# Kernel tuning notes

Hardware: AMD Instinct MI355X
Metric: run time of the kernel (lower is better)

## Reference

```python
import jax, jax.numpy as jnp
import numpy as np

B, T, W, H = 4, 4096, 1024, 8
BW = W // H  # block width


@jax.custom_vjp
def sqrt_bound(x):
    return jnp.sqrt(x)

def _sb_fwd(x):
    return jnp.sqrt(x), x

def _sb_bwd(x, g):
    return (g / jnp.sqrt(jnp.clip(4.0 * x, 1e-6)),)

sqrt_bound.defvjp(_sb_fwd, _sb_bwd)


def block_diag_linear(x, w, b):
    # x: [B,T,W] -> [B,T,H,BW]; w: [H,BW,BW]; b: [H,BW]
    xb = x.reshape(x.shape[0], x.shape[1], H, BW)
    y = jnp.einsum('bthi,hij->bthj', xb, w) + b
    return y.reshape(x.shape)


def setup_inputs() -> dict:
    key = jax.random.key(0)
    k1, k2, k3, k4 = jax.random.split(key, 4)
    x = jax.random.normal(k1, (B, T, W), dtype=jnp.float32)
    segment_pos = jnp.broadcast_to(jnp.arange(T, dtype=jnp.int32)[None, :], (B, T))
    std = 1.0 / np.sqrt(BW)
    w_in = std * jax.random.normal(k2, (H, BW, BW), dtype=jnp.float32)
    b_in = jnp.zeros((H, BW), dtype=jnp.float32)
    w_a = std * jax.random.normal(k3, (H, BW, BW), dtype=jnp.float32)
    b_a = jnp.zeros((H, BW), dtype=jnp.float32)
    # rnn_param_init: a_param = log(u^{-0.5} - 1), u ~ U(min_rad^2+eps, max_rad^2+eps)
    u = jax.random.uniform(k4, (W,), dtype=jnp.float32,
                           minval=0.9 ** 2 + 1e-8, maxval=0.999 ** 2 + 1e-8)
    a_param = jnp.log(jnp.exp(-0.5 * jnp.log(u)) - 1.0)
    return {'x': x, 'segment_pos': segment_pos, 'a_param': a_param,
            'w_in': w_in, 'b_in': b_in, 'w_a': w_a, 'b_a': b_a}


def reference(x, segment_pos, a_param, w_in, b_in, w_a, b_a):
    gate_x = jax.nn.sigmoid(block_diag_linear(x, w_in, b_in))
    gate_a = jax.nn.sigmoid(block_diag_linear(x, w_a, b_a))
    log_a = -8.0 * gate_a * jax.nn.softplus(a_param)  # [B,T,W]
    a = jnp.exp(log_a)
    multiplier = sqrt_bound(1.0 - jnp.exp(2.0 * log_a))
    normed_x = x * gate_x * multiplier
    reset = (segment_pos == 0)  # [B,T] bool
    a_eff = a * (~reset)[..., None].astype(a.dtype)
    # diagonal linear recurrence h_t = a_t * h_{t-1} + x_t via lax.scan over time
    def step(h, inp):
        a_t, x_t = inp
        h = a_t * h + x_t
        return h, h
    xs = (jnp.swapaxes(a_eff, 0, 1), jnp.swapaxes(normed_x, 0, 1))  # [T,B,W]
    h0 = jnp.zeros((x.shape[0], x.shape[2]), dtype=x.dtype)
    _, ys = jax.lax.scan(step, h0, xs)
    return jnp.swapaxes(ys, 0, 1)  # [B,T,W]
```

## Files before the change

kernel.cpp:

```cpp
#include <hip/hip_runtime.h>
#include <math.h>

#define NB 4
#define NT 4096
#define NW 1024
#define NH 8
#define CHUNK 64
#define NCH 64
#define STRIDE_A 136

typedef __attribute__((ext_vector_type(8))) short short8;
typedef __attribute__((ext_vector_type(4))) float f32x4;

__device__ __forceinline__ short bf16rne(float f) {
    unsigned u = __float_as_uint(f);
    u += 0x7fffu + ((u >> 16) & 1u);
    return (short)(u >> 16);
}

__global__ __launch_bounds__(256)
void k0_wfrag(const float* __restrict__ w_in, const float* __restrict__ w_a,
              short* __restrict__ wfH)
{
    int idx = blockIdx.x * 256 + threadIdx.x;
    int j4 = (idx & 31) * 4;
    int i  = (idx >> 5) & 127;
    int h  = (idx >> 12) & 7;
    int g  = idx >> 15;
    const float* w = g ? w_a : w_in;
    float4 v = *(const float4*)&w[((size_t)h * 128 + i) * 128 + j4];
    const float vf[4] = {v.x, v.y, v.z, v.w};
    const int ks = i >> 5, q = (i >> 3) & 3, jj = i & 7;
    #pragma unroll
    for (int d = 0; d < 4; ++d) {
        int j = j4 + d;
        int lane = q * 16 + (j & 15);
        int ntg = j >> 4;
        size_t dst = ((size_t)(((h * 2 + g) * 4 + ks) * 8 + ntg) * 64 + lane) * 8 + jj;
        wfH[dst] = bf16rne(vf[d]);
    }
}

__global__ __launch_bounds__(512)
void k_pass(const float* __restrict__ x, const int* __restrict__ seg,
            const float* __restrict__ a_param,
            const float* __restrict__ b_in, const float* __restrict__ b_a,
            const short* __restrict__ wfH,
            const float* __restrict__ Hst,
            float* __restrict__ Atop, float* __restrict__ Htop,
            float* __restrict__ out, const int final_pass)
{
    __shared__ short sA[64 * STRIDE_A];

    const int h   = blockIdx.x;
    const int bc  = blockIdx.y;
    const int b   = bc >> 6, c = bc & 63;
    const int tid = threadIdx.x;
    const int wave = tid >> 6, lane = tid & 63;
    const int quad = lane >> 4, m = lane & 15;
    const int row0 = b * NT + c * CHUNK;

    {
        const int r  = tid >> 3;
        const int k0 = (tid & 7) * 16;
        const float4* px = (const float4*)(x + (size_t)(row0 + r) * NW + h * 128 + k0);
        float4 v0 = px[0], v1 = px[1], v2 = px[2], v3 = px[3];
        const float f[16] = {v0.x, v0.y, v0.z, v0.w, v1.x, v1.y, v1.z, v1.w,
                             v2.x, v2.y, v2.z, v2.w, v3.x, v3.y, v3.z, v3.w};
        short8 s0, s1;
        #pragma unroll
        for (int j = 0; j < 8; ++j) { s0[j] = bf16rne(f[j]); s1[j] = bf16rne(f[8 + j]); }
        *(short8*)&sA[r * STRIDE_A + k0]     = s0;
        *(short8*)&sA[r * STRIDE_A + k0 + 8] = s1;
    }
    __syncthreads();

    f32x4 acc[2][4];
    #pragma unroll
    for (int g = 0; g < 2; ++g)
        #pragma unroll
        for (int mt = 0; mt < 4; ++mt)
            acc[g][mt] = (f32x4){0.f, 0.f, 0.f, 0.f};

    #pragma unroll
    for (int ks = 0; ks < 4; ++ks) {
        short8 ah[4];
        #pragma unroll
        for (int mt = 0; mt < 4; ++mt)
            ah[mt] = *(const short8*)&sA[(mt * 16 + m) * STRIDE_A + ks * 32 + quad * 8];
        #pragma unroll
        for (int g = 0; g < 2; ++g) {
            const size_t fo = ((size_t)(((h * 2 + g) * 4 + ks) * 8 + wave) * 64 + lane) * 8;
            short8 bh = *(const short8*)(wfH + fo);
            #pragma unroll
            for (int mt = 0; mt < 4; ++mt)
                acc[g][mt] = __builtin_amdgcn_mfma_f32_16x16x32_bf16(ah[mt], bh, acc[g][mt], 0, 0, 0);
        }
    }

    const int col  = wave * 16 + m;
    const int colg = h * 128 + col;
    const float bi = b_in[colg];
    const float ba = b_a[colg];
    const float c2 = -8.0f * log1pf(expf(a_param[colg]));
    const size_t topbase = ((size_t)(h * NB + b) * NCH + c) * 128;
    const float hprev = final_pass ? Hst[topbase + col] : 0.f;

    float cA = 1.f, cH = 0.f;
    for (int mt = 0; mt < 4; ++mt) {
        float lP[4], lH[4];
        {
            float xv[4]; int sv[4];
            #pragma unroll
            for (int r = 0; r < 4; ++r) {
                const int rowi = row0 + mt * 16 + quad * 4 + r;
                xv[r] = x[(size_t)rowi * NW + colg];
                sv[r] = seg[rowi];
            }
            #pragma unroll
            for (int r = 0; r < 4; ++r) {
                const float zx = acc[0][mt][r] + bi;
                const float za = acc[1][mt][r] + ba;
                const float gx = __fdividef(1.f, 1.f + __expf(-zx));
                const float ga = __fdividef(1.f, 1.f + __expf(-za));
                const float a  = __expf(c2 * ga);
                const float mult = sqrtf(fmaxf(fmaf(-a, a, 1.f), 0.f));
                const float av = (sv[r] == 0) ? 0.f : a;
                const float nx = xv[r] * gx * mult;
                lP[r] = (r == 0) ? av : lP[r - 1] * av;
                lH[r] = (r == 0) ? nx : fmaf(av, lH[r - 1], nx);
            }
        }
        float iA = lP[3], iH = lH[3];
        float uA = __shfl_up(iA, 16), uH = __shfl_up(iH, 16);
        if (quad >= 1) { iH = fmaf(iA, uH, iH); iA = uA * iA; }
        uA = __shfl_up(iA, 32); uH = __shfl_up(iH, 32);
        if (quad >= 2) { iH = fmaf(iA, uH, iH); iA = uA * iA; }
        float eA = __shfl_up(iA, 16), eH = __shfl_up(iH, 16);
        if (quad == 0) { eA = 1.f; eH = 0.f; }
        const float mAt = __shfl(iA, 48 + m);
        const float mHt = __shfl(iH, 48 + m);
        const float pA = cA * eA;
        const float pH = fmaf(eA, cH, eH);
        cH = fmaf(mAt, cH, mHt);
        cA = cA * mAt;
        if (final_pass) {
            #pragma unroll
            for (int r = 0; r < 4; ++r) {
                const int rowi = row0 + mt * 16 + quad * 4 + r;
                const float Pf = pA * lP[r];
                const float Hf = fmaf(lP[r], pH, lH[r]);
                out[(size_t)rowi * NW + colg] = fmaf(Pf, hprev, Hf);
            }
        }
    }
    if (!final_pass && quad == 0) {
        Atop[topbase + col] = cA;
        Htop[topbase + col] = cH;
    }
}

__global__ __launch_bounds__(256)
void k3_tops(const float* __restrict__ Atop, const float* __restrict__ Htop,
             float* __restrict__ Hst)
{
    const int idx = blockIdx.x * 256 + threadIdx.x;
    const int col = idx & 127;
    const int hb  = idx >> 7;
    const size_t base = (size_t)hb * NCH * 128 + col;
    float hh = 0.f;
    #pragma unroll 16
    for (int cc = 0; cc < NCH; ++cc) {
        const size_t o = base + (size_t)cc * 128;
        Hst[o] = hh;
        hh = fmaf(Atop[o], hh, Htop[o]);
    }
}

extern "C" void kernel_launch(void* const* d_in, const int* in_sizes, int n_in,
                              void* d_out, int out_size, void* d_ws, size_t ws_size,
                              hipStream_t stream)
{
    (void)in_sizes; (void)n_in; (void)out_size; (void)ws_size;
    const float* x    = (const float*)d_in[0];
    const int*   seg  = (const int*)  d_in[1];
    const float* ap   = (const float*)d_in[2];
    const float* w_in = (const float*)d_in[3];
    const float* b_in = (const float*)d_in[4];
    const float* w_a  = (const float*)d_in[5];
    const float* b_a  = (const float*)d_in[6];
    float* out = (float*)d_out;

    const size_t NTOP = (size_t)NH * NB * NCH * 128;
    float* Atop = (float*)d_ws;
    float* Htop = Atop + NTOP;
    float* Hst  = Htop + NTOP;
    short* wfH  = (short*)(Hst + NTOP);

    k0_wfrag<<<256, 256, 0, stream>>>(w_in, w_a, wfH);
    dim3 g1(NH, NB * NCH);
    k_pass<<<g1, 512, 0, stream>>>(x, seg, ap, b_in, b_a, wfH, Hst,
                                   Atop, Htop, out, 0);
    k3_tops<<<(NH * NB * 128) / 256, 256, 0, stream>>>(Atop, Htop, Hst);
    k_pass<<<g1, 512, 0, stream>>>(x, seg, ap, b_in, b_a, wfH, Hst,
                                   Atop, Htop, out, 1);
}
```

Before: 187.5 us.

## Fuse two-pass chunked scan into single pass with decoupled look-back

Replaces the two-pass scheme (local chunk scan, serial tops scan, then a recompute pass) with one fused kernel. Each chunk publishes its aggregate (A, H) and inclusive prefix, and the next chunks look back through predecessors using NaN-poisoned flags, which the weight-prep kernel initialises. This drops the recomputation of the GEMM and gates and the extra launches, so x is read only once. In exchange it relies on inter-block spin-waiting with relaxed atomics, which could stall or deadlock if later chunks are scheduled before earlier ones. It also lacks acquire/release ordering between the separate flag stores.

```diff
diff --git a/kernel.cpp b/kernel.cpp
--- a/kernel.cpp
+++ b/kernel.cpp
@@ -20,9 +20,14 @@
 
 __global__ __launch_bounds__(256)
 void k0_wfrag(const float* __restrict__ w_in, const float* __restrict__ w_a,
-              short* __restrict__ wfH)
+              short* __restrict__ wfH, uint4* __restrict__ poison)
 {
     int idx = blockIdx.x * 256 + threadIdx.x;
+    uint4 nv; nv.x = nv.y = nv.z = nv.w = 0xFFFFFFFFu;
+    poison[idx]          = nv;
+    poison[idx + 65536]  = nv;
+    poison[idx + 131072] = nv;
+
     int j4 = (idx & 31) * 4;
     int i  = (idx >> 5) & 127;
     int h  = (idx >> 12) & 7;
@@ -42,13 +47,12 @@
 }
 
 __global__ __launch_bounds__(512)
-void k_pass(const float* __restrict__ x, const int* __restrict__ seg,
-            const float* __restrict__ a_param,
-            const float* __restrict__ b_in, const float* __restrict__ b_a,
-            const short* __restrict__ wfH,
-            const float* __restrict__ Hst,
-            float* __restrict__ Atop, float* __restrict__ Htop,
-            float* __restrict__ out, const int final_pass)
+void k_fused(const float* __restrict__ x, const int* __restrict__ seg,
+             const float* __restrict__ a_param,
+             const float* __restrict__ b_in, const float* __restrict__ b_a,
+             const short* __restrict__ wfH,
+             float* __restrict__ Ag, float* __restrict__ Hg,
+             float* __restrict__ Hi, float* __restrict__ out)
 {
     __shared__ short sA[64 * STRIDE_A];
 
@@ -103,10 +107,10 @@
     const float bi = b_in[colg];
     const float ba = b_a[colg];
     const float c2 = -8.0f * log1pf(expf(a_param[colg]));
-    const size_t topbase = ((size_t)(h * NB + b) * NCH + c) * 128;
-    const float hprev = final_pass ? Hst[topbase + col] : 0.f;
 
     float cA = 1.f, cH = 0.f;
+    float Pf[4][4], Hf[4][4];
+    #pragma unroll
     for (int mt = 0; mt < 4; ++mt) {
         float lP[4], lH[4];
         {
@@ -144,36 +148,51 @@
         const float pH = fmaf(eA, cH, eH);
         cH = fmaf(mAt, cH, mHt);
         cA = cA * mAt;
-        if (final_pass) {
-            #pragma unroll
-            for (int r = 0; r < 4; ++r) {
-                const int rowi = row0 + mt * 16 + quad * 4 + r;
-                const float Pf = pA * lP[r];
-                const float Hf = fmaf(lP[r], pH, lH[r]);
-                out[(size_t)rowi * NW + colg] = fmaf(Pf, hprev, Hf);
+        #pragma unroll
+        for (int r = 0; r < 4; ++r) {
+            Pf[mt][r] = pA * lP[r];
+            Hf[mt][r] = fmaf(lP[r], pH, lH[r]);
+        }
+    }
+
+    const size_t cb0 = (size_t)(h * NB + b) * NCH * 128;
+    float hp = 0.f;
+    if (quad == 0) {
+        const size_t oc = cb0 + (size_t)c * 128 + col;
+        if (c > 0) {
+            __hip_atomic_store(&Ag[oc], cA, __ATOMIC_RELAXED, __HIP_MEMORY_SCOPE_AGENT);
+            __hip_atomic_store(&Hg[oc], cH, __ATOMIC_RELAXED, __HIP_MEMORY_SCOPE_AGENT);
+            float accA = 1.f, accH = 0.f;
+            int k = c - 1;
+            for (;;) {
+                const size_t o = cb0 + (size_t)k * 128 + col;
+                const float hv = __hip_atomic_load(&Hi[o], __ATOMIC_RELAXED, __HIP_MEMORY_SCOPE_AGENT);
+                const float A_ = __hip_atomic_load(&Ag[o], __ATOMIC_RELAXED, __HIP_MEMORY_SCOPE_AGENT);
+                const float H_ = __hip_atomic_load(&Hg[o], __ATOMIC_RELAXED, __HIP_MEMORY_SCOPE_AGENT);
+                if (!__builtin_isnan(hv)) {
+                    hp = fmaf(accA, hv, accH);
+                    break;
+                }
+                if (__builtin_isnan(A_) || __builtin_isnan(H_)) {
+                    __builtin_amdgcn_s_sleep(2);
+                    continue;
+                }
+                accH = fmaf(accA, H_, accH);
+                accA *= A_;
+                --k;
             }
         }
-    }
-    if (!final_pass && quad == 0) {
-        Atop[topbase + col] = cA;
-        Htop[topbase + col] = cH;
-    }
-}
-
-__global__ __launch_bounds__(256)
-void k3_tops(const float* __restrict__ Atop, const float* __restrict__ Htop,
-             float* __restrict__ Hst)
-{
-    const int idx = blockIdx.x * 256 + threadIdx.x;
-    const int col = idx & 127;
-    const int hb  = idx >> 7;
-    const size_t base = (size_t)hb * NCH * 128 + col;
-    float hh = 0.f;
-    #pragma unroll 16
-    for (int cc = 0; cc < NCH; ++cc) {
-        const size_t o = base + (size_t)cc * 128;
-        Hst[o] = hh;
-        hh = fmaf(Atop[o], hh, Htop[o]);
+        __hip_atomic_store(&Hi[oc], fmaf(cA, hp, cH), __ATOMIC_RELAXED, __HIP_MEMORY_SCOPE_AGENT);
+    }
+    hp = __shfl(hp, m);
+
+    #pragma unroll
+    for (int mt = 0; mt < 4; ++mt) {
+        #pragma unroll
+        for (int r = 0; r < 4; ++r) {
+            const int rowi = row0 + mt * 16 + quad * 4 + r;
+            out[(size_t)rowi * NW + colg] = fmaf(Pf[mt][r], hp, Hf[mt][r]);
+        }
     }
 }
 
@@ -192,16 +211,12 @@
     float* out = (float*)d_out;
 
     const size_t NTOP = (size_t)NH * NB * NCH * 128;
-    float* Atop = (float*)d_ws;
-    float* Htop = Atop + NTOP;
-    float* Hst  = Htop + NTOP;
-    short* wfH  = (short*)(Hst + NTOP);
-
-    k0_wfrag<<<256, 256, 0, stream>>>(w_in, w_a, wfH);
+    float* Ag  = (float*)d_ws;
+    float* Hg  = Ag + NTOP;
+    float* Hi  = Hg + NTOP;
+    short* wfH = (short*)(Hi + NTOP);
+
+    k0_wfrag<<<256, 256, 0, stream>>>(w_in, w_a, wfH, (uint4*)Ag);
     dim3 g1(NH, NB * NCH);
-    k_pass<<<g1, 512, 0, stream>>>(x, seg, ap, b_in, b_a, wfH, Hst,
-                                   Atop, Htop, out, 0);
-    k3_tops<<<(NH * NB * 128) / 256, 256, 0, stream>>>(Atop, Htop, Hst);
-    k_pass<<<g1, 512, 0, stream>>>(x, seg, ap, b_in, b_a, wfH, Hst,
-                                   Atop, Htop, out, 1);
-}
+    k_fused<<<g1, 512, 0, stream>>>(x, seg, ap, b_in, b_a, wfH, Ag, Hg, Hi, out);
+}
```

New measurement: 159.9 us. -14.7%, faster.
